# Optimization experiments

Measured on AMD Instinct MI355X. Metric: run time of the kernel, lower is better.

The kernel has to match this reference:

```python
import jax, jax.numpy as jnp
import numpy as np

N = 300000        # occupied voxels
G = 128           # voxel grid side
C_IN = 128
C_OUT = 32
TIMES = C_IN // C_OUT
K = 27            # 3^3 kernel offsets


def _build_kernel_map():
    """Sample N unique voxels in a G^3 grid and build the 27-offset neighbor map.
    nbr[k, n] = index of the voxel at coords[n] + offset[k], or N if absent."""
    rng = np.random.default_rng(0)
    lin = rng.choice(G ** 3, size=N, replace=False).astype(np.int64)
    coords = np.stack(np.unravel_index(lin, (G, G, G)), axis=1).astype(np.int64)  # [N,3]
    lookup = np.full(G ** 3, N, dtype=np.int32)
    lookup[lin] = np.arange(N, dtype=np.int32)
    offs = np.stack(np.meshgrid(*[[-1, 0, 1]] * 3, indexing='ij'), axis=-1).reshape(-1, 3)  # [27,3]
    nbr = np.empty((K, N), dtype=np.int32)
    for k, off in enumerate(offs):
        nc = coords + off
        valid = np.all((nc >= 0) & (nc < G), axis=1)
        li = (nc[:, 0] * G + nc[:, 1]) * G + nc[:, 2]
        nbr[k] = np.where(valid, lookup[np.clip(li, 0, G ** 3 - 1)], N)
    return nbr


def setup_inputs() -> dict:
    key = jax.random.key(0)
    k1, k2, k3, k4 = jax.random.split(key, 4)
    feats = jax.random.normal(k1, (N, C_IN), dtype=jnp.float32)
    W0 = jax.random.normal(k2, (K, C_IN, C_IN), dtype=jnp.float32) * 0.05
    W1 = jax.random.normal(k3, (K, C_IN, C_OUT), dtype=jnp.float32) * 0.05
    W2 = jax.random.normal(k4, (K, C_OUT, C_OUT), dtype=jnp.float32) * 0.05
    nbr_idx = jnp.asarray(_build_kernel_map())
    return {"feats": feats, "W0": W0, "W1": W1, "W2": W2, "nbr_idx": nbr_idx}


def sparse_conv(x, W, nbr):
    """Gather-GEMM-accumulate sparse conv: out[n] = sum_k x[nbr[k,n]] @ W[k].
    Missing neighbors (index N) gather a zero row."""
    xp = jnp.concatenate([x, jnp.zeros((1, x.shape[1]), x.dtype)], axis=0)  # [N+1,Cin]
    out0 = jnp.zeros((x.shape[0], W.shape[2]), x.dtype)

    def body(acc, kw):
        idx, Wk = kw
        return acc + xp[idx] @ Wk, None

    out, _ = jax.lax.scan(body, out0, (nbr, W))
    return out


def reference(feats, W0, W1, W2, nbr_idx):
    n = feats.shape[0]
    # mean over channel groups: [N, times, C_out] -> [N, C_out]
    downsampled = jnp.mean(feats.reshape(n, TIMES, C_OUT), axis=1)
    upsampled = jnp.tile(downsampled, (1, TIMES))           # [N, C_in]
    residual = feats - upsampled
    residual = sparse_conv(residual, W0, nbr_idx)           # C_in -> C_in
    residual = sparse_conv(residual, W1, nbr_idx)           # C_in -> C_out
    residual = sparse_conv(residual, W2, nbr_idx)           # C_out -> C_out
    return downsampled + residual
```

## Files before the change

kernel.cpp:

```cpp
#include <hip/hip_runtime.h>

#define DEVINL __device__ __forceinline__

typedef __attribute__((ext_vector_type(8))) __bf16 bf16x8;
typedef __attribute__((ext_vector_type(4))) float f32x4;
typedef __attribute__((ext_vector_type(8))) unsigned short u16x8;

DEVINL unsigned short f2bf(float x) {
  unsigned u = __builtin_bit_cast(unsigned, x);
  u += 0x7FFFu + ((u >> 16) & 1u);
  return (unsigned short)(u >> 16);
}

#define BARRIER() asm volatile("s_barrier" ::: "memory")

template <int N>
DEVINL void waitvm() {
  asm volatile("s_waitcnt vmcnt(%0)" ::"n"(N) : "memory");
}

DEVINL void gload16(const void* g, void* l) {
  __builtin_amdgcn_global_load_lds(
      (const __attribute__((address_space(1))) void*)g,
      (__attribute__((address_space(3))) void*)l, 16, 0, 0);
}

__global__ __launch_bounds__(256) void prep_kernel(
    const float* __restrict__ F, unsigned short* __restrict__ RES,
    float* __restrict__ DS, int n) {
  const int t = threadIdx.x;
  const int row = blockIdx.x * 16 + (t >> 4);
  const int cg = t & 15;
  if (row >= n) return;
  const float4* f4 = (const float4*)(F + (size_t)row * 128 + cg * 8);
  float4 v0 = f4[0], v1 = f4[1];
  float v[8] = {v0.x, v0.y, v0.z, v0.w, v1.x, v1.y, v1.z, v1.w};
  float s[8] = {v0.x, v0.y, v0.z, v0.w, v1.x, v1.y, v1.z, v1.w};
#pragma unroll
  for (int i = 0; i < 8; ++i) s[i] += __shfl_xor(s[i], 4);
#pragma unroll
  for (int i = 0; i < 8; ++i) s[i] += __shfl_xor(s[i], 8);
  u16x8 rb;
#pragma unroll
  for (int i = 0; i < 8; ++i) rb[i] = f2bf(v[i] - 0.25f * s[i]);
  *(u16x8*)(RES + (size_t)row * 128 + cg * 8) = rb;
  if (cg < 4) {
    float4 d0 = {0.25f * s[0], 0.25f * s[1], 0.25f * s[2], 0.25f * s[3]};
    float4 d1 = {0.25f * s[4], 0.25f * s[5], 0.25f * s[6], 0.25f * s[7]};
    float4* dp = (float4*)(DS + (size_t)row * 32 + cg * 8);
    dp[0] = d0;
    dp[1] = d1;
  }
}

template <int CIN, int COUT>
DEVINL void pack_one(const float* __restrict__ W, unsigned short* __restrict__ P, int g) {
  const int n = g % COUT;
  const int t = g / COUT;
  const int q = t & 3;
  const int t2 = t >> 2;
  const int ks = t2 % (CIN / 32);
  const int k = t2 / (CIN / 32);
  const float* src = W + ((size_t)k * CIN + ks * 32 + q * 8) * COUT + n;
  unsigned short* dst = P + (size_t)g * 8;
#pragma unroll
  for (int j = 0; j < 8; ++j) dst[j] = f2bf(src[(size_t)j * COUT]);
}

__global__ __launch_bounds__(256) void pack_kernel(
    const float* __restrict__ W0, const float* __restrict__ W1,
    const float* __restrict__ W2, unsigned short* __restrict__ P0,
    unsigned short* __restrict__ P1, unsigned short* __restrict__ P2) {
  int g = blockIdx.x * 256 + threadIdx.x;
  if (g < 55296)
    pack_one<128, 128>(W0, P0, g);
  else if (g < 69120)
    pack_one<128, 32>(W1, P1, g - 55296);
  else if (g < 72576)
    pack_one<32, 32>(W2, P2, g - 69120);
}

__global__ void zero_tail(unsigned short* a, unsigned short* b, unsigned short* c) {
  int t = threadIdx.x;
  if (t < 128) { a[t] = 0; b[t] = 0; }
  if (t < 32) c[t] = 0;
}

template <int CIN, int COUT, int BK, int BM, int PF, int WM, int WN, bool FINAL,
          int MINB>
__global__ __launch_bounds__(256, MINB) void spconv(
    const unsigned short* __restrict__ X, const unsigned short* __restrict__ Bp,
    const int* __restrict__ nbr, unsigned short* __restrict__ Y,
    float* __restrict__ OUT, const float* __restrict__ DS, int nr) {
  constexpr int H = CIN / BK;
  constexpr int S = 27 * H;
  constexpr int NBUF = PF + 1;
  constexpr int KSL = BK / 32;
  constexpr int WROWS = BM / WM;
  constexpr int WCOLS = COUT / WN;
  constexpr int MF = WROWS / 16;
  constexpr int NF = WCOLS / 16;
  constexpr int CPR = BK / 8;
  constexpr int SWZ = (CPR < 8 ? CPR - 1 : 7);
  constexpr int RB = BK * 2;
  constexpr int APF = BM * CPR / 256;
  constexpr int NB = KSL * NF;

  __shared__ unsigned short As[NBUF][BM * BK];
  __shared__ int IdxS[28 * BM];

  const int tid = threadIdx.x;
  const int lane = tid & 63;
  const int wave = tid >> 6;
  const int wm = wave / WN;
  const int wn = wave % WN;
  const int base = blockIdx.x * BM;
  const int q = lane >> 4;
  const int l16 = lane & 15;

  for (int f = tid; f < 28 * BM; f += 256) {
    int k = f / BM;
    int nn = base + (f % BM);
    IdxS[f] = (k < 27 && nn < nr) ? nbr[(size_t)k * nr + nn] : nr;
  }
  __syncthreads();

  const unsigned short* bbase = Bp + ((size_t)q * COUT + wn * WCOLS + l16) * 8;

  bf16x8 bA[NB], bB[NB];

  auto loadB = [&](bf16x8(&dst)[NB], int s) {
    const int k0 = s / H;
    const int k = (k0 > 26) ? 26 : k0;
    const int hh = s % H;
#pragma unroll
    for (int ks = 0; ks < KSL; ++ks)
#pragma unroll
      for (int j = 0; j < NF; ++j) {
        const int ksg = hh * KSL + ks;
        dst[ks * NF + j] = *(const bf16x8*)(
            bbase + ((size_t)k * CIN * COUT) + ((size_t)(ksg * 4) * COUT + j * 16) * 8);
      }
  };

  auto issueA = [&](int s) {
    const int k = s / H;
    const int hh = s % H;
    const int kb = s % NBUF;
#pragma unroll
    for (int pp = 0; pp < APF; ++pp) {
      int slot = pp * 256 + tid;
      int r = slot / CPR;
      int cc = (slot % CPR) * 16;
      int csw = cc ^ ((r & SWZ) << 4);
      int g = IdxS[k * BM + r];
      gload16(X + (size_t)g * CIN + hh * BK + (csw >> 1),
              (char*)(&As[kb][0]) + slot * 16);
    }
  };

  f32x4 acc[MF][NF] = {};

  auto mfmaStep = [&](int kb, const bf16x8(&bf)[NB]) {
    const char* Ab = (const char*)(&As[kb][0]);
#pragma unroll
    for (int ks = 0; ks < KSL; ++ks) {
      bf16x8 af[MF];
#pragma unroll
      for (int i = 0; i < MF; ++i) {
        int r = wm * WROWS + i * 16 + l16;
        int db = r * RB + (((ks * 64 + q * 16) & (RB - 1)) ^ ((r & SWZ) << 4));
        af[i] = __builtin_bit_cast(bf16x8, *(const uint4*)(Ab + db));
      }
#pragma unroll
      for (int i = 0; i < MF; ++i)
#pragma unroll
        for (int j = 0; j < NF; ++j)
          acc[i][j] = __builtin_amdgcn_mfma_f32_16x16x32_bf16(af[i], bf[ks * NF + j],
                                                              acc[i][j], 0, 0, 0);
    }
  };

  issueA(0);
  loadB(bA, 0);
  if constexpr (PF >= 2) issueA(1);

#pragma unroll 1
  for (int s = 0; s + 1 < S; s += 2) {
    loadB(bB, s + 1);
    issueA(s + PF);
    waitvm<NB + PF * APF>();
    BARRIER();
    mfmaStep(s % NBUF, bA);
    BARRIER();
    loadB(bA, s + 2);
    issueA(s + 1 + PF);
    waitvm<NB + PF * APF>();
    BARRIER();
    mfmaStep((s + 1) % NBUF, bB);
    BARRIER();
  }
  waitvm<0>();
  if constexpr (S & 1) {
    BARRIER();
    mfmaStep((S - 1) % NBUF, bA);
  }

#pragma unroll
  for (int i = 0; i < MF; ++i)
#pragma unroll
    for (int j = 0; j < NF; ++j)
#pragma unroll
      for (int r = 0; r < 4; ++r) {
        int row = base + wm * WROWS + i * 16 + q * 4 + r;
        int col = wn * WCOLS + j * 16 + l16;
        if (row < nr) {
          float v = acc[i][j][r];
          if constexpr (FINAL)
            OUT[(size_t)row * COUT + col] = v + DS[(size_t)row * COUT + col];
          else
            Y[(size_t)row * COUT + col] = f2bf(v);
        }
      }
}

extern "C" void kernel_launch(void* const* d_in, const int* in_sizes, int n_in,
                              void* d_out, int out_size, void* d_ws, size_t ws_size,
                              hipStream_t stream) {
  const float* feats = (const float*)d_in[0];
  const float* W0 = (const float*)d_in[1];
  const float* W1 = (const float*)d_in[2];
  const float* W2 = (const float*)d_in[3];
  const int* nbr = (const int*)d_in[4];
  const int n = in_sizes[0] / 128;
  float* out = (float*)d_out;

  char* p = (char*)d_ws;
  auto take = [&](size_t bytes) {
    char* r = p;
    p += (bytes + 255) & ~(size_t)255;
    return r;
  };
  unsigned short* resB = (unsigned short*)take((size_t)(n + 1) * 128 * 2);
  unsigned short* y0 = (unsigned short*)take((size_t)(n + 1) * 128 * 2);
  unsigned short* y1 = (unsigned short*)take((size_t)(n + 1) * 32 * 2);
  float* ds = (float*)take((size_t)n * 32 * 4);
  unsigned short* p0 = (unsigned short*)take((size_t)27 * 128 * 128 * 2);
  unsigned short* p1 = (unsigned short*)take((size_t)27 * 128 * 32 * 2);
  unsigned short* p2 = (unsigned short*)take((size_t)27 * 32 * 32 * 2);

  prep_kernel<<<(n + 15) / 16, 256, 0, stream>>>(feats, resB, ds, n);
  pack_kernel<<<284, 256, 0, stream>>>(W0, W1, W2, p0, p1, p2);
  zero_tail<<<1, 128, 0, stream>>>(resB + (size_t)n * 128, y0 + (size_t)n * 128,
                                   y1 + (size_t)n * 32);
  const int gb128 = (n + 127) / 128;
  spconv<128, 128, 64, 128, 1, 2, 2, false, 2>
      <<<gb128, 256, 0, stream>>>(resB, p0, nbr, y0, nullptr, nullptr, n);
  spconv<128, 32, 64, 128, 1, 4, 1, false, 3>
      <<<gb128, 256, 0, stream>>>(y0, p1, nbr, y1, nullptr, nullptr, n);
  spconv<32, 32, 32, 128, 1, 4, 1, true, 4>
      <<<gb128, 256, 0, stream>>>(y1, p2, nbr, nullptr, out, ds, n);
}
```

Before: 531.1 us.

## Gather A rows directly into registers for narrow-output convs, rebalance first conv waves

Adds a spconv_reg variant that loads gathered neighbor rows straight from global memory into registers instead of staging them in LDS through global_load_lds, and uses it for the second and third convolutions, whose wave layout gives each wave distinct rows with no A-tile sharing. This drops the LDS traffic and the extra barriers around staging. The first convolution changes its wave layout from 2x2 to 1x4 and raises the occupancy hint from 2 to 3. The cost is more register pressure, and in the first conv each wave now covers all 128 rows, so it reads more A fragments from LDS.

```diff
diff --git a/kernel.cpp b/kernel.cpp
--- a/kernel.cpp
+++ b/kernel.cpp
@@ -224,6 +224,124 @@
       }
 }
 
+template <int CIN, int COUT, int BK, int BM, int WM, int WN, bool FINAL, int MINB>
+__global__ __launch_bounds__(256, MINB) void spconv_reg(
+    const unsigned short* __restrict__ X, const unsigned short* __restrict__ Bp,
+    const int* __restrict__ nbr, unsigned short* __restrict__ Y,
+    float* __restrict__ OUT, const float* __restrict__ DS, int nr) {
+  constexpr int H = CIN / BK;
+  constexpr int S = 27 * H;
+  constexpr int KSL = BK / 32;
+  constexpr int WROWS = BM / WM;
+  constexpr int WCOLS = COUT / WN;
+  constexpr int MF = WROWS / 16;
+  constexpr int NF = WCOLS / 16;
+  constexpr int NB = KSL * NF;
+  constexpr int AL = MF * KSL;
+
+  __shared__ int IdxS[28 * BM];
+
+  const int tid = threadIdx.x;
+  const int lane = tid & 63;
+  const int wave = tid >> 6;
+  const int wm = wave / WN;
+  const int wn = wave % WN;
+  const int base = blockIdx.x * BM;
+  const int q = lane >> 4;
+  const int l16 = lane & 15;
+
+  for (int f = tid; f < 28 * BM; f += 256) {
+    int k = f / BM;
+    int nn = base + (f % BM);
+    IdxS[f] = (k < 27 && nn < nr) ? nbr[(size_t)k * nr + nn] : nr;
+  }
+  __syncthreads();
+
+  const unsigned short* bbase = Bp + ((size_t)q * COUT + wn * WCOLS + l16) * 8;
+
+  bf16x8 bA[NB], bB[NB], aA[AL], aB[AL];
+
+  auto loadB = [&](bf16x8(&dst)[NB], int s) {
+    const int k0 = s / H;
+    const int k = (k0 > 26) ? 26 : k0;
+    const int hh = s % H;
+#pragma unroll
+    for (int ks = 0; ks < KSL; ++ks)
+#pragma unroll
+      for (int j = 0; j < NF; ++j) {
+        const int ksg = hh * KSL + ks;
+        dst[ks * NF + j] = *(const bf16x8*)(
+            bbase + ((size_t)k * CIN * COUT) + ((size_t)(ksg * 4) * COUT + j * 16) * 8);
+      }
+  };
+
+  auto loadA = [&](bf16x8(&dst)[AL], int s) {
+    const int k = s / H;
+    const int hh = s % H;
+#pragma unroll
+    for (int i = 0; i < MF; ++i) {
+      int r = wm * WROWS + i * 16 + l16;
+      int g = IdxS[k * BM + r];
+      const unsigned short* src = X + (size_t)g * CIN + hh * BK + q * 8;
+#pragma unroll
+      for (int ks = 0; ks < KSL; ++ks)
+        dst[i * KSL + ks] = *(const bf16x8*)(src + ks * 32);
+    }
+  };
+
+  f32x4 acc[MF][NF] = {};
+
+  auto mfmaStep = [&](const bf16x8(&af)[AL], const bf16x8(&bf)[NB]) {
+#pragma unroll
+    for (int ks = 0; ks < KSL; ++ks)
+#pragma unroll
+      for (int i = 0; i < MF; ++i)
+#pragma unroll
+        for (int j = 0; j < NF; ++j)
+          acc[i][j] = __builtin_amdgcn_mfma_f32_16x16x32_bf16(
+              af[i * KSL + ks], bf[ks * NF + j], acc[i][j], 0, 0, 0);
+  };
+
+  loadB(bA, 0);
+  loadA(aA, 0);
+
+#pragma unroll 1
+  for (int s = 0; s + 1 < S; s += 2) {
+    loadB(bB, s + 1);
+    loadA(aB, s + 1);
+    waitvm<NB + AL>();
+    BARRIER();
+    mfmaStep(aA, bA);
+    loadB(bA, s + 2);
+    loadA(aA, s + 2);
+    waitvm<NB + AL>();
+    BARRIER();
+    mfmaStep(aB, bB);
+  }
+  if constexpr (S & 1) {
+    waitvm<0>();
+    BARRIER();
+    mfmaStep(aA, bA);
+  }
+
+#pragma unroll
+  for (int i = 0; i < MF; ++i)
+#pragma unroll
+    for (int j = 0; j < NF; ++j)
+#pragma unroll
+      for (int r = 0; r < 4; ++r) {
+        int row = base + wm * WROWS + i * 16 + q * 4 + r;
+        int col = wn * WCOLS + j * 16 + l16;
+        if (row < nr) {
+          float v = acc[i][j][r];
+          if constexpr (FINAL)
+            OUT[(size_t)row * COUT + col] = v + DS[(size_t)row * COUT + col];
+          else
+            Y[(size_t)row * COUT + col] = f2bf(v);
+        }
+      }
+}
+
 extern "C" void kernel_launch(void* const* d_in, const int* in_sizes, int n_in,
                               void* d_out, int out_size, void* d_ws, size_t ws_size,
                               hipStream_t stream) {
@@ -254,10 +372,10 @@
   zero_tail<<<1, 128, 0, stream>>>(resB + (size_t)n * 128, y0 + (size_t)n * 128,
                                    y1 + (size_t)n * 32);
   const int gb128 = (n + 127) / 128;
-  spconv<128, 128, 64, 128, 1, 2, 2, false, 2>
+  spconv<128, 128, 64, 128, 1, 1, 4, false, 3>
       <<<gb128, 256, 0, stream>>>(resB, p0, nbr, y0, nullptr, nullptr, n);
-  spconv<128, 32, 64, 128, 1, 4, 1, false, 3>
+  spconv_reg<128, 32, 64, 128, 4, 1, false, 3>
       <<<gb128, 256, 0, stream>>>(y0, p1, nbr, y1, nullptr, nullptr, n);
-  spconv<32, 32, 32, 128, 1, 4, 1, true, 4>
+  spconv_reg<32, 32, 32, 128, 4, 1, true, 4>
       <<<gb128, 256, 0, stream>>>(y1, p2, nbr, nullptr, out, ds, n);
 }
```

Result: faster. 509.1 us (median of 2 runs) (-4.1%).
